# Kernel optimization log

Hardware: AMD Instinct MI355X
Metric: run time of the kernel (lower is better)

Reference implementation:

```python
import jax, jax.numpy as jnp
import numpy as np

# ---- static problem dims (mirror the Triton kernel's constexprs) ----
NUM_SEQS = 2
LQ = 1024            # query tokens per sequence (uniform varlen instance)
HIST = 1024          # cached-prefix length per sequence
LK = LQ + HIST       # total kv length per sequence
NUM_HEADS = 32
NUM_KV_HEADS = 8
HEAD_DIM = 128
BLOCK_SIZE = 64
MAX_NUM_BLOCKS = LK // BLOCK_SIZE          # 32 logical blocks per sequence
TOTAL_BLOCKS = NUM_SEQS * MAX_NUM_BLOCKS   # physical blocks in the cache
NEG = -1e10                                # matches kernel's -10000000000.0


def setup_inputs() -> dict:
    key = jax.random.key(0)
    k1, k2, k3, k4 = jax.random.split(key, 4)
    q = jax.random.normal(k1, (NUM_SEQS * LQ, NUM_HEADS, HEAD_DIM), jnp.float32)
    k_cache = jax.random.normal(k2, (TOTAL_BLOCKS, BLOCK_SIZE, NUM_KV_HEADS, HEAD_DIM), jnp.float32)
    v_cache = jax.random.normal(k3, (TOTAL_BLOCKS, BLOCK_SIZE, NUM_KV_HEADS, HEAD_DIM), jnp.float32)
    cu_seqlens_q = (jnp.arange(NUM_SEQS + 1, dtype=jnp.int32) * LQ)
    cu_seqlens_k = (jnp.arange(NUM_SEQS + 1, dtype=jnp.int32) * LK)
    # scattered physical block layout: a random permutation -> irregular gather
    block_tables = jax.random.permutation(k4, TOTAL_BLOCKS).astype(jnp.int32).reshape(NUM_SEQS, MAX_NUM_BLOCKS)
    return dict(q=q, k_cache=k_cache, v_cache=v_cache,
                cu_seqlens_q=cu_seqlens_q, cu_seqlens_k=cu_seqlens_k,
                block_tables=block_tables)


def _paged_prefill_attention(q, k_cache, v_cache, cu_seqlens_q, cu_seqlens_k, block_tables):
    scale = 1.0 / np.sqrt(HEAD_DIM)
    seq_len_q = cu_seqlens_q[1:] - cu_seqlens_q[:-1]            # [S]
    seq_len_k = cu_seqlens_k[1:] - cu_seqlens_k[:-1]            # [S]
    history_len = seq_len_k - seq_len_q                          # [S]

    # uniform varlen instance: flat [total_q, H, D] -> [S, LQ, H, D]
    qr = q.reshape(NUM_SEQS, LQ, NUM_HEADS, HEAD_DIM)
    group = NUM_HEADS // NUM_KV_HEADS
    # [S, LQ, KVH, G, D] so head h maps to kv head h // group (kernel's kv_head_idx)
    q5 = qr.reshape(NUM_SEQS, LQ, NUM_KV_HEADS, group, HEAD_DIM) * scale

    # block-table gather: logical kv layout per sequence
    safe_tables = jnp.maximum(block_tables, 0)
    k = k_cache[safe_tables].reshape(NUM_SEQS, LK, NUM_KV_HEADS, HEAD_DIM)
    v = v_cache[safe_tables].reshape(NUM_SEQS, LK, NUM_KV_HEADS, HEAD_DIM)

    # scores [S, KVH, G, LQ, LK]
    scores = jnp.einsum('sqhgd,skhd->shgqk', q5, k)

    pos_q = jnp.arange(LQ, dtype=jnp.int32)[None, :] + history_len[:, None]   # [S, LQ] absolute positions
    pos_k = jnp.arange(LK, dtype=jnp.int32)                                   # [LK]
    valid_k = (pos_k[None, :] < seq_len_k[:, None]) & \
              jnp.repeat(block_tables >= 0, BLOCK_SIZE, axis=1)               # [S, LK]
    causal = pos_q[:, :, None] >= pos_k[None, None, :]                        # [S, LQ, LK]
    mask = causal & valid_k[:, None, :]
    scores = jnp.where(mask[:, None, None, :, :], scores, NEG)

    p = jax.nn.softmax(scores, axis=-1)  # online-softmax in kernel == exact softmax
    out = jnp.einsum('shgqk,skhd->sqhgd', p, v)
    return out.reshape(NUM_SEQS * LQ, NUM_HEADS, HEAD_DIM)


def reference(q, k_cache, v_cache, cu_seqlens_q, cu_seqlens_k, block_tables):
    return _paged_prefill_attention(q, k_cache, v_cache, cu_seqlens_q, cu_seqlens_k, block_tables)
```

## Files before the change

### kernel.cpp

```cpp
#include <hip/hip_runtime.h>
#include <hip/hip_bf16.h>

#define NS_    2
#define LQ_    1024
#define HIST_  1024
#define LK_    2048
#define NH_    32
#define NKVH_  8
#define HD_    128
#define BS_    64
#define BM_    128
#define MAXB_  32

typedef __attribute__((ext_vector_type(8))) short short8;
typedef __attribute__((ext_vector_type(4))) float f32x4;

#define VSTR 72

static __device__ __forceinline__ unsigned short f2bf(float x) {
    __hip_bfloat16 h = __float2bfloat16(x);
    return *(unsigned short*)&h;
}

static __device__ __forceinline__ void cp16(const void* g, void* l) {
    __builtin_amdgcn_global_load_lds(
        (const __attribute__((address_space(1))) void*)g,
        (__attribute__((address_space(3))) void*)l, 16, 0, 0);
}

template<int CTRL>
static __device__ __forceinline__ float dppmax(float x) {
    int y = __builtin_amdgcn_update_dpp(0, __float_as_int(x), CTRL, 0xf, 0xf, true);
    return fmaxf(x, __int_as_float(y));
}

__global__ __launch_bounds__(256)
void prep_kv(const float* __restrict__ kc, const float* __restrict__ vc,
             const int* __restrict__ bt,
             unsigned short* __restrict__ Kb, unsigned short* __restrict__ Vb)
{
    __shared__ __align__(16) unsigned short Vt[HD_ * VSTR];
    const int tid = threadIdx.x;
    const int gid = blockIdx.x & 511;
    const int seq = gid >> 8;
    const int kvh = (gid >> 5) & 7;
    const int blk = gid & 31;
    const int ph  = bt[seq * MAXB_ + blk];
    const size_t src = ((size_t)ph * BS_ * NKVH_ + kvh) * HD_;
    const int grp = seq * NKVH_ + kvh;

    if (blockIdx.x < 512) {
        const int t8 = tid >> 5, kq = tid & 31;
#pragma unroll
        for (int p = 0; p < 8; ++p) {
            const int tok = p * 8 + t8;
            float4 f = *(const float4*)(kc + src + (size_t)tok * (NKVH_ * HD_) + kq * 4);
            unsigned short u[4] = {f2bf(f.x), f2bf(f.y), f2bf(f.z), f2bf(f.w)};
            *(uint2*)(Kb + ((size_t)grp * LK_ + blk * BS_ + tok) * HD_ + kq * 4) = *(const uint2*)u;
        }
    } else {
        const int e8 = tid >> 5, dq = tid & 31;
        float4 vr[8];
#pragma unroll
        for (int j = 0; j < 8; ++j)
            vr[j] = *(const float4*)(vc + src + (size_t)(e8 * 8 + j) * (NKVH_ * HD_) + dq * 4);
#pragma unroll
        for (int w2 = 0; w2 < 4; ++w2) {
            unsigned short row[8];
#pragma unroll
            for (int j = 0; j < 8; ++j) {
                float f = (w2 == 0) ? vr[j].x : (w2 == 1) ? vr[j].y : (w2 == 2) ? vr[j].z : vr[j].w;
                row[j] = f2bf(f);
            }
            *(short8*)&Vt[(dq * 4 + w2) * VSTR + e8 * 8] = *(const short8*)row;
        }
        __syncthreads();
#pragma unroll
        for (int u = 0; u < 4; ++u) {
            const int c  = tid + 256 * u;
            const int d  = c >> 3, ch = c & 7;
            uint4 x = *(const uint4*)&Vt[d * VSTR + ch * 8];
            *(uint4*)(Vb + ((size_t)grp * HD_ + d) * LK_ + blk * BS_ + ch * 8) = x;
        }
    }
}

template<bool PREP>
__global__ __launch_bounds__(256, 2)
void paged_attn(const float* __restrict__ q,
                const unsigned short* __restrict__ Kb,
                const unsigned short* __restrict__ Vb,
                const float* __restrict__ kc,
                const float* __restrict__ vc,
                const int* __restrict__ bt,
                float* __restrict__ out)
{
    __shared__ __align__(16) unsigned short Ksh[BS_ * HD_];
    __shared__ __align__(16) unsigned short Vsh[HD_ * BS_];
    __shared__ __align__(16) unsigned short Psh[BM_ * BS_];

    const int tid  = threadIdx.x;
    const int w    = tid >> 6;
    const int lane = tid & 63;
    const int n    = lane & 15;
    const int q4   = lane >> 4;

    const int gid  = blockIdx.x;
    const int kvh  = gid & 7;
    const int slot = gid >> 3;
    const int seq  = slot >> 5;
    const int sub  = slot & 31;
    const int head = kvh * 4 + (sub & 3);
    const int m0   = (sub >> 2) * BM_;
    const int r0   = m0 + w * 32;
    const int grp  = seq * NKVH_ + kvh;

    short8 qf[2][4];
#pragma unroll
    for (int rt = 0; rt < 2; ++rt) {
        const size_t base = ((size_t)((seq * LQ_ + r0 + rt * 16 + n) * NH_ + head)) * HD_;
#pragma unroll
        for (int c = 0; c < 4; ++c) {
            float4 a = *(const float4*)(q + base + c * 32 + q4 * 8);
            float4 b = *(const float4*)(q + base + c * 32 + q4 * 8 + 4);
            unsigned short u[8] = {f2bf(a.x), f2bf(a.y), f2bf(a.z), f2bf(a.w),
                                   f2bf(b.x), f2bf(b.y), f2bf(b.z), f2bf(b.w)};
            qf[rt][c] = *(const short8*)u;
        }
    }

    f32x4 acc[2][8];
    f32x4 lf[2];
    float mrow[2][4];
#pragma unroll
    for (int rt = 0; rt < 2; ++rt) {
        lf[rt] = (f32x4){0.f, 0.f, 0.f, 0.f};
#pragma unroll
        for (int dt = 0; dt < 8; ++dt) acc[rt][dt] = (f32x4){0.f, 0.f, 0.f, 0.f};
#pragma unroll
        for (int r = 0; r < 4; ++r) mrow[rt][r] = -1e30f;
    }

    const int nb = (HIST_ + m0 + BM_ - 1) / BS_ + 1;
    const float SC = 0.08838834764831845f * 1.4426950408889634f;

    for (int b = 0; b < nb; ++b) {
        __syncthreads();
        if constexpr (PREP) {
            const size_t kg = ((size_t)grp * LK_ + b * BS_) * HD_;
#pragma unroll
            for (int j = 0; j < 4; ++j) {
                const int row = w * 16 + j * 4 + (lane >> 4);
                const int c8  = (lane & 15) ^ (row & 15);
                cp16(Kb + kg + (size_t)row * HD_ + c8 * 8, &Ksh[(w * 16 + j * 4) * HD_]);
            }
            const size_t vg = (size_t)grp * HD_ * LK_ + b * BS_;
#pragma unroll
            for (int j = 0; j < 4; ++j) {
                const int d  = w * 32 + j * 8 + (lane >> 3);
                const int c8 = (lane & 7) ^ (d & 7);
                cp16(Vb + vg + (size_t)d * LK_ + c8 * 8, &Vsh[(w * 32 + j * 8) * BS_]);
            }
        } else {
            const int ph = bt[seq * MAXB_ + b];
            const size_t src = ((size_t)ph * BS_ * NKVH_ + kvh) * HD_;
#pragma unroll
            for (int j = 0; j < 4; ++j) {
                const int row = w * 16 + j * 4 + (lane >> 4);
                const int c8  = (lane & 15) ^ (row & 15);
                float4 a = *(const float4*)(kc + src + (size_t)row * (NKVH_ * HD_) + c8 * 8);
                float4 b2 = *(const float4*)(kc + src + (size_t)row * (NKVH_ * HD_) + c8 * 8 + 4);
                unsigned short u[8] = {f2bf(a.x), f2bf(a.y), f2bf(a.z), f2bf(a.w),
                                       f2bf(b2.x), f2bf(b2.y), f2bf(b2.z), f2bf(b2.w)};
                *(short8*)&Ksh[row * HD_ + (lane & 15) * 8] = *(const short8*)u;
            }
#pragma unroll
            for (int j = 0; j < 4; ++j) {
                const int d  = w * 32 + j * 8 + (lane >> 3);
                const int c8 = (lane & 7) ^ (d & 7);
                unsigned short u[8];
#pragma unroll
                for (int i2 = 0; i2 < 8; ++i2)
                    u[i2] = f2bf(vc[src + (size_t)(c8 * 8 + i2) * (NKVH_ * HD_) + d]);
                *(short8*)&Vsh[d * BS_ + (lane & 7) * 8] = *(const short8*)u;
            }
        }
        __syncthreads();

        if (64 * b <= HIST_ + r0 + 31) {
            f32x4 s[2][4];
#pragma unroll
            for (int rt = 0; rt < 2; ++rt)
#pragma unroll
                for (int kt = 0; kt < 4; ++kt) s[rt][kt] = (f32x4){0.f, 0.f, 0.f, 0.f};
#pragma unroll
            for (int kt = 0; kt < 4; ++kt) {
#pragma unroll
                for (int c = 0; c < 4; ++c) {
                    short8 kf = *(const short8*)&Ksh[(kt * 16 + n) * HD_ + (((c * 4 + q4) ^ n) << 3)];
#pragma unroll
                    for (int rt = 0; rt < 2; ++rt)
                        s[rt][kt] = __builtin_amdgcn_mfma_f32_16x16x32_bf16(qf[rt][c], kf, s[rt][kt], 0, 0, 0);
                }
            }
            const bool needMask = (64 * b + 63 > HIST_ + r0);
#pragma unroll
            for (int rt = 0; rt < 2; ++rt) {
                float mx[4], al[4];
#pragma unroll
                for (int r = 0; r < 4; ++r) mx[r] = -1e30f;
#pragma unroll
                for (int kt = 0; kt < 4; ++kt) {
#pragma unroll
                    for (int r = 0; r < 4; ++r) {
                        float t = s[rt][kt][r] * SC;
                        if (needMask) {
                            const int key = b * 64 + kt * 16 + n;
                            const int row = r0 + rt * 16 + q4 * 4 + r;
                            if (key > HIST_ + row) t = -1e30f;
                        }
                        s[rt][kt][r] = t;
                        mx[r] = fmaxf(mx[r], t);
                    }
                }
#pragma unroll
                for (int r = 0; r < 4; ++r) {
                    mx[r] = dppmax<0xB1>(mx[r]);
                    mx[r] = dppmax<0x4E>(mx[r]);
                    mx[r] = dppmax<0x124>(mx[r]);
                    mx[r] = dppmax<0x128>(mx[r]);
                    const float mn = fmaxf(mrow[rt][r], mx[r]);
                    al[r] = __builtin_amdgcn_exp2f(mrow[rt][r] - mn);
                    mrow[rt][r] = mn;
                }
                const int rbase = w * 32 + rt * 16 + q4 * 4;
#pragma unroll
                for (int kt = 0; kt < 4; ++kt) {
                    const int cb = kt * 2 + (n >> 3);
                    const int ci = n & 7;
#pragma unroll
                    for (int r = 0; r < 4; ++r) {
                        const int row = rbase + r;
                        const float p = __builtin_amdgcn_exp2f(s[rt][kt][r] - mrow[rt][r]);
                        Psh[row * BS_ + ((cb ^ (row & 7)) << 3) + ci] = f2bf(p);
                    }
                }
                if (__any(al[0] != 1.f || al[1] != 1.f || al[2] != 1.f || al[3] != 1.f)) {
#pragma unroll
                    for (int dt = 0; dt < 8; ++dt)
#pragma unroll
                        for (int r = 0; r < 4; ++r) acc[rt][dt][r] *= al[r];
#pragma unroll
                    for (int r = 0; r < 4; ++r) lf[rt][r] *= al[r];
                }
            }
            short8 ones;
#pragma unroll
            for (int j = 0; j < 8; ++j) ones[j] = (short)0x3F80;
#pragma unroll
            for (int ks = 0; ks < 2; ++ks) {
                short8 pa[2];
#pragma unroll
                for (int rt = 0; rt < 2; ++rt)
                    pa[rt] = *(const short8*)&Psh[(w * 32 + rt * 16 + n) * BS_ + (((ks * 4 + q4) ^ (n & 7)) << 3)];
#pragma unroll
                for (int rt = 0; rt < 2; ++rt)
                    lf[rt] = __builtin_amdgcn_mfma_f32_16x16x32_bf16(pa[rt], ones, lf[rt], 0, 0, 0);
#pragma unroll
                for (int dt = 0; dt < 8; ++dt) {
                    short8 vf = *(const short8*)&Vsh[(dt * 16 + n) * BS_ + (((ks * 4 + q4) ^ (n & 7)) << 3)];
#pragma unroll
                    for (int rt = 0; rt < 2; ++rt)
                        acc[rt][dt] = __builtin_amdgcn_mfma_f32_16x16x32_bf16(pa[rt], vf, acc[rt][dt], 0, 0, 0);
                }
            }
        }
    }

#pragma unroll
    for (int rt = 0; rt < 2; ++rt) {
        float rl[4];
#pragma unroll
        for (int r = 0; r < 4; ++r) rl[r] = 1.0f / lf[rt][r];
#pragma unroll
        for (int dt = 0; dt < 8; ++dt)
#pragma unroll
            for (int r = 0; r < 4; ++r) {
                const int row = r0 + rt * 16 + q4 * 4 + r;
                out[((size_t)((seq * LQ_ + row) * NH_ + head)) * HD_ + dt * 16 + n] = acc[rt][dt][r] * rl[r];
            }
    }
}

extern "C" void kernel_launch(void* const* d_in, const int* in_sizes, int n_in,
                              void* d_out, int out_size, void* d_ws, size_t ws_size,
                              hipStream_t stream) {
    const float* q  = (const float*)d_in[0];
    const float* kc = (const float*)d_in[1];
    const float* vc = (const float*)d_in[2];
    const int*   bt = (const int*)d_in[5];
    float*      out = (float*)d_out;
    (void)in_sizes; (void)n_in; (void)out_size;

    const size_t kb_elems = (size_t)NS_ * NKVH_ * LK_ * HD_;
    const size_t need = kb_elems * 2 * sizeof(unsigned short);
    if (ws_size >= need) {
        unsigned short* Kb = (unsigned short*)d_ws;
        unsigned short* Vb = Kb + kb_elems;
        prep_kv<<<1024, 256, 0, stream>>>(kc, vc, bt, Kb, Vb);
        paged_attn<true><<<512, 256, 0, stream>>>(q, Kb, Vb, kc, vc, bt, out);
    } else {
        paged_attn<false><<<512, 256, 0, stream>>>(q, nullptr, nullptr, kc, vc, bt, out);
    }
}
```

Measured before the change: 208.7 us.

## Double-buffer K/V tiles, balance causal tiles, fold scale into Q, merge prep

```diff
diff --git a/kernel.cpp b/kernel.cpp
--- a/kernel.cpp
+++ b/kernel.cpp
@@ -41,47 +41,45 @@
 {
     __shared__ __align__(16) unsigned short Vt[HD_ * VSTR];
     const int tid = threadIdx.x;
-    const int gid = blockIdx.x & 511;
+    const int gid = blockIdx.x;
     const int seq = gid >> 8;
     const int kvh = (gid >> 5) & 7;
     const int blk = gid & 31;
     const int ph  = bt[seq * MAXB_ + blk];
     const size_t src = ((size_t)ph * BS_ * NKVH_ + kvh) * HD_;
     const int grp = seq * NKVH_ + kvh;
-
-    if (blockIdx.x < 512) {
-        const int t8 = tid >> 5, kq = tid & 31;
-#pragma unroll
-        for (int p = 0; p < 8; ++p) {
-            const int tok = p * 8 + t8;
-            float4 f = *(const float4*)(kc + src + (size_t)tok * (NKVH_ * HD_) + kq * 4);
-            unsigned short u[4] = {f2bf(f.x), f2bf(f.y), f2bf(f.z), f2bf(f.w)};
-            *(uint2*)(Kb + ((size_t)grp * LK_ + blk * BS_ + tok) * HD_ + kq * 4) = *(const uint2*)u;
-        }
-    } else {
-        const int e8 = tid >> 5, dq = tid & 31;
-        float4 vr[8];
-#pragma unroll
-        for (int j = 0; j < 8; ++j)
-            vr[j] = *(const float4*)(vc + src + (size_t)(e8 * 8 + j) * (NKVH_ * HD_) + dq * 4);
-#pragma unroll
-        for (int w2 = 0; w2 < 4; ++w2) {
-            unsigned short row[8];
-#pragma unroll
-            for (int j = 0; j < 8; ++j) {
-                float f = (w2 == 0) ? vr[j].x : (w2 == 1) ? vr[j].y : (w2 == 2) ? vr[j].z : vr[j].w;
-                row[j] = f2bf(f);
-            }
-            *(short8*)&Vt[(dq * 4 + w2) * VSTR + e8 * 8] = *(const short8*)row;
-        }
-        __syncthreads();
-#pragma unroll
-        for (int u = 0; u < 4; ++u) {
-            const int c  = tid + 256 * u;
-            const int d  = c >> 3, ch = c & 7;
-            uint4 x = *(const uint4*)&Vt[d * VSTR + ch * 8];
-            *(uint4*)(Vb + ((size_t)grp * HD_ + d) * LK_ + blk * BS_ + ch * 8) = x;
-        }
+    const int t8 = tid >> 5, q32 = tid & 31;
+
+    float4 kr[8], vr[8];
+#pragma unroll
+    for (int p = 0; p < 8; ++p)
+        kr[p] = *(const float4*)(kc + src + (size_t)(p * 8 + t8) * (NKVH_ * HD_) + q32 * 4);
+#pragma unroll
+    for (int j = 0; j < 8; ++j)
+        vr[j] = *(const float4*)(vc + src + (size_t)(t8 * 8 + j) * (NKVH_ * HD_) + q32 * 4);
+
+#pragma unroll
+    for (int p = 0; p < 8; ++p) {
+        unsigned short u[4] = {f2bf(kr[p].x), f2bf(kr[p].y), f2bf(kr[p].z), f2bf(kr[p].w)};
+        *(uint2*)(Kb + ((size_t)grp * LK_ + blk * BS_ + p * 8 + t8) * HD_ + q32 * 4) = *(const uint2*)u;
+    }
+#pragma unroll
+    for (int w2 = 0; w2 < 4; ++w2) {
+        unsigned short row[8];
+#pragma unroll
+        for (int j = 0; j < 8; ++j) {
+            float f = (w2 == 0) ? vr[j].x : (w2 == 1) ? vr[j].y : (w2 == 2) ? vr[j].z : vr[j].w;
+            row[j] = f2bf(f);
+        }
+        *(short8*)&Vt[(q32 * 4 + w2) * VSTR + t8 * 8] = *(const short8*)row;
+    }
+    __syncthreads();
+#pragma unroll
+    for (int u = 0; u < 4; ++u) {
+        const int c  = tid + 256 * u;
+        const int d  = c >> 3, ch = c & 7;
+        uint4 x = *(const uint4*)&Vt[d * VSTR + ch * 8];
+        *(uint4*)(Vb + ((size_t)grp * HD_ + d) * LK_ + blk * BS_ + ch * 8) = x;
     }
 }
 
@@ -95,8 +93,8 @@
                 const int* __restrict__ bt,
                 float* __restrict__ out)
 {
-    __shared__ __align__(16) unsigned short Ksh[BS_ * HD_];
-    __shared__ __align__(16) unsigned short Vsh[HD_ * BS_];
+    __shared__ __align__(16) unsigned short Ksh[2][BS_ * HD_];
+    __shared__ __align__(16) unsigned short Vsh[2][HD_ * BS_];
     __shared__ __align__(16) unsigned short Psh[BM_ * BS_];
 
     const int tid  = threadIdx.x;
@@ -110,11 +108,15 @@
     const int slot = gid >> 3;
     const int seq  = slot >> 5;
     const int sub  = slot & 31;
-    const int head = kvh * 4 + (sub & 3);
-    const int m0   = (sub >> 2) * BM_;
+    const int e    = sub & 1;
+    const int t3   = (sub >> 1) & 7;
+    const int hp   = sub >> 4;
+    const int head = kvh * 4 + hp * 2 + e;
+    const int m0   = (e ? (7 - t3) : t3) * BM_;
     const int r0   = m0 + w * 32;
     const int grp  = seq * NKVH_ + kvh;
 
+    const float SC = 0.08838834764831845f * 1.4426950408889634f;
     short8 qf[2][4];
 #pragma unroll
     for (int rt = 0; rt < 2; ++rt) {
@@ -123,8 +125,8 @@
         for (int c = 0; c < 4; ++c) {
             float4 a = *(const float4*)(q + base + c * 32 + q4 * 8);
             float4 b = *(const float4*)(q + base + c * 32 + q4 * 8 + 4);
-            unsigned short u[8] = {f2bf(a.x), f2bf(a.y), f2bf(a.z), f2bf(a.w),
-                                   f2bf(b.x), f2bf(b.y), f2bf(b.z), f2bf(b.w)};
+            unsigned short u[8] = {f2bf(a.x * SC), f2bf(a.y * SC), f2bf(a.z * SC), f2bf(a.w * SC),
+                                   f2bf(b.x * SC), f2bf(b.y * SC), f2bf(b.z * SC), f2bf(b.w * SC)};
             qf[rt][c] = *(const short8*)u;
         }
     }
@@ -142,25 +144,39 @@
     }
 
     const int nb = (HIST_ + m0 + BM_ - 1) / BS_ + 1;
-    const float SC = 0.08838834764831845f * 1.4426950408889634f;
+    const unsigned short* kSrc = Kb + (size_t)grp * LK_ * HD_;
+    const unsigned short* vSrc = Vb + (size_t)grp * HD_ * LK_;
+
+    const int krow_ = w * 16 + (lane >> 4);
+    const int kc8_  = ((lane & 15) ^ (krow_ & 15));
+    const int vd_   = w * 32 + (lane >> 3);
+    const int vc8_  = ((lane & 7) ^ (vd_ & 7));
+
+    auto issue = [&](int b, int buf) {
+#pragma unroll
+        for (int j = 0; j < 4; ++j) {
+            const int row = krow_ + j * 4;
+            const int c8  = (lane & 15) ^ (row & 15);
+            cp16(kSrc + ((size_t)b * BS_ + row) * HD_ + c8 * 8, &Ksh[buf][(w * 16 + j * 4) * HD_]);
+        }
+#pragma unroll
+        for (int j = 0; j < 4; ++j) {
+            const int d  = vd_ + j * 8;
+            const int c8 = (lane & 7) ^ (d & 7);
+            cp16(vSrc + (size_t)d * LK_ + b * BS_ + c8 * 8, &Vsh[buf][(w * 32 + j * 8) * BS_]);
+        }
+    };
+
+    if constexpr (PREP) issue(0, 0);
+    short8 ones;
+#pragma unroll
+    for (int j = 0; j < 8; ++j) ones[j] = (short)0x3F80;
 
     for (int b = 0; b < nb; ++b) {
+        const int cur = PREP ? (b & 1) : 0;
         __syncthreads();
         if constexpr (PREP) {
-            const size_t kg = ((size_t)grp * LK_ + b * BS_) * HD_;
-#pragma unroll
-            for (int j = 0; j < 4; ++j) {
-                const int row = w * 16 + j * 4 + (lane >> 4);
-                const int c8  = (lane & 15) ^ (row & 15);
-                cp16(Kb + kg + (size_t)row * HD_ + c8 * 8, &Ksh[(w * 16 + j * 4) * HD_]);
-            }
-            const size_t vg = (size_t)grp * HD_ * LK_ + b * BS_;
-#pragma unroll
-            for (int j = 0; j < 4; ++j) {
-                const int d  = w * 32 + j * 8 + (lane >> 3);
-                const int c8 = (lane & 7) ^ (d & 7);
-                cp16(Vb + vg + (size_t)d * LK_ + c8 * 8, &Vsh[(w * 32 + j * 8) * BS_]);
-            }
+            if (b + 1 < nb) issue(b + 1, 1 ^ cur);
         } else {
             const int ph = bt[seq * MAXB_ + b];
             const size_t src = ((size_t)ph * BS_ * NKVH_ + kvh) * HD_;
@@ -172,7 +188,7 @@
                 float4 b2 = *(const float4*)(kc + src + (size_t)row * (NKVH_ * HD_) + c8 * 8 + 4);
                 unsigned short u[8] = {f2bf(a.x), f2bf(a.y), f2bf(a.z), f2bf(a.w),
                                        f2bf(b2.x), f2bf(b2.y), f2bf(b2.z), f2bf(b2.w)};
-                *(short8*)&Ksh[row * HD_ + (lane & 15) * 8] = *(const short8*)u;
+                *(short8*)&Ksh[0][row * HD_ + (lane & 15) * 8] = *(const short8*)u;
             }
 #pragma unroll
             for (int j = 0; j < 4; ++j) {
@@ -182,10 +198,10 @@
 #pragma unroll
                 for (int i2 = 0; i2 < 8; ++i2)
                     u[i2] = f2bf(vc[src + (size_t)(c8 * 8 + i2) * (NKVH_ * HD_) + d]);
-                *(short8*)&Vsh[d * BS_ + (lane & 7) * 8] = *(const short8*)u;
-            }
-        }
-        __syncthreads();
+                *(short8*)&Vsh[0][d * BS_ + (lane & 7) * 8] = *(const short8*)u;
+            }
+            __syncthreads();
+        }
 
         if (64 * b <= HIST_ + r0 + 31) {
             f32x4 s[2][4];
@@ -197,7 +213,7 @@
             for (int kt = 0; kt < 4; ++kt) {
 #pragma unroll
                 for (int c = 0; c < 4; ++c) {
-                    short8 kf = *(const short8*)&Ksh[(kt * 16 + n) * HD_ + (((c * 4 + q4) ^ n) << 3)];
+                    short8 kf = *(const short8*)&Ksh[cur][(kt * 16 + n) * HD_ + (((c * 4 + q4) ^ n) << 3)];
 #pragma unroll
                     for (int rt = 0; rt < 2; ++rt)
                         s[rt][kt] = __builtin_amdgcn_mfma_f32_16x16x32_bf16(qf[rt][c], kf, s[rt][kt], 0, 0, 0);
@@ -213,7 +229,7 @@
                 for (int kt = 0; kt < 4; ++kt) {
 #pragma unroll
                     for (int r = 0; r < 4; ++r) {
-                        float t = s[rt][kt][r] * SC;
+                        float t = s[rt][kt][r];
                         if (needMask) {
                             const int key = b * 64 + kt * 16 + n;
                             const int row = r0 + rt * 16 + q4 * 4 + r;
@@ -254,9 +270,6 @@
                     for (int r = 0; r < 4; ++r) lf[rt][r] *= al[r];
                 }
             }
-            short8 ones;
-#pragma unroll
-            for (int j = 0; j < 8; ++j) ones[j] = (short)0x3F80;
 #pragma unroll
             for (int ks = 0; ks < 2; ++ks) {
                 short8 pa[2];
@@ -268,7 +281,7 @@
                     lf[rt] = __builtin_amdgcn_mfma_f32_16x16x32_bf16(pa[rt], ones, lf[rt], 0, 0, 0);
 #pragma unroll
                 for (int dt = 0; dt < 8; ++dt) {
-                    short8 vf = *(const short8*)&Vsh[(dt * 16 + n) * BS_ + (((ks * 4 + q4) ^ (n & 7)) << 3)];
+                    short8 vf = *(const short8*)&Vsh[cur][(dt * 16 + n) * BS_ + (((ks * 4 + q4) ^ (n & 7)) << 3)];
 #pragma unroll
                     for (int rt = 0; rt < 2; ++rt)
                         acc[rt][dt] = __builtin_amdgcn_mfma_f32_16x16x32_bf16(pa[rt], vf, acc[rt][dt], 0, 0, 0);
@@ -307,7 +320,7 @@
     if (ws_size >= need) {
         unsigned short* Kb = (unsigned short*)d_ws;
         unsigned short* Vb = Kb + kb_elems;
-        prep_kv<<<1024, 256, 0, stream>>>(kc, vc, bt, Kb, Vb);
+        prep_kv<<<512, 256, 0, stream>>>(kc, vc, bt, Kb, Vb);
         paged_attn<true><<<512, 256, 0, stream>>>(q, Kb, Vb, kc, vc, bt, out);
     } else {
         paged_attn<false><<<512, 256, 0, stream>>>(q, nullptr, nullptr, kc, vc, bt, out);
```

After: 207.9 us. About the same (-0.4%).
